# Kernel tuning notes

Measured on AMD Instinct MI355X. Metric: run time of the kernel, lower is better.

Reference implementation:

```python
import jax, jax.numpy as jnp
import numpy as np

N = 50000
E = 1600000
IN_CH = 128
HID = 32
HEADS = 4
NEG_SLOPE = 0.2
BN_EPS = 1e-5


def _gat_layer(x, src, dst, W, att_src, att_dst, n):
    """PyG-style GATConv (no bias; bias added by caller).
    x: [n, f_in], W: [f_in, heads*out], att_*: [heads, out].
    Returns [n, heads, out]."""
    heads, out_ch = att_src.shape
    h = (x @ W).reshape(n, heads, out_ch)                 # node projections
    a_s = jnp.einsum('nhc,hc->nh', h, att_src)            # per-node src logit
    a_d = jnp.einsum('nhc,hc->nh', h, att_dst)            # per-node dst logit
    e = jax.nn.leaky_relu(a_s[src] + a_d[dst], NEG_SLOPE)  # [E_tot, heads]
    m = jax.ops.segment_max(e, dst, num_segments=n)       # per-target max (stable softmax)
    ex = jnp.exp(e - m[dst])
    denom = jax.ops.segment_sum(ex, dst, num_segments=n)
    alpha = ex / denom[dst]                               # segment softmax over incoming edges
    out = jax.ops.segment_sum(h[src] * alpha[:, :, None], dst, num_segments=n)
    return out


def setup_inputs():
    key = jax.random.key(0)
    ks = jax.random.split(key, 8)
    x = jax.random.normal(ks[0], (N, IN_CH), dtype=jnp.float32)
    edge_index = jax.random.randint(ks[1], (2, E), 0, N, dtype=jnp.int32)
    s1 = 1.0 / float(np.sqrt(IN_CH))
    W1 = jax.random.uniform(ks[2], (IN_CH, HEADS * HID), jnp.float32, -s1, s1)
    att_src1 = jax.random.uniform(ks[3], (HEADS, HID), jnp.float32, -s1, s1)
    att_dst1 = jax.random.uniform(ks[4], (HEADS, HID), jnp.float32, -s1, s1)
    bias1 = jnp.zeros((HEADS * HID,), jnp.float32)
    bn_gamma = jnp.ones((HEADS * HID,), jnp.float32)
    bn_beta = jnp.zeros((HEADS * HID,), jnp.float32)
    bn_mean = jnp.zeros((HEADS * HID,), jnp.float32)
    bn_var = jnp.ones((HEADS * HID,), jnp.float32)
    s2 = 1.0 / float(np.sqrt(HEADS * HID))
    W2 = jax.random.uniform(ks[5], (HEADS * HID, 2), jnp.float32, -s2, s2)
    att_src2 = jax.random.uniform(ks[6], (1, 2), jnp.float32, -s2, s2)
    att_dst2 = jax.random.uniform(ks[7], (1, 2), jnp.float32, -s2, s2)
    bias2 = jnp.zeros((2,), jnp.float32)
    return {"x": x, "edge_index": edge_index, "W1": W1, "att_src1": att_src1,
            "att_dst1": att_dst1, "bias1": bias1, "bn_gamma": bn_gamma,
            "bn_beta": bn_beta, "bn_mean": bn_mean, "bn_var": bn_var,
            "W2": W2, "att_src2": att_src2, "att_dst2": att_dst2, "bias2": bias2}


def reference(x, edge_index, W1, att_src1, att_dst1, bias1, bn_gamma, bn_beta,
              bn_mean, bn_var, W2, att_src2, att_dst2, bias2):
    n = x.shape[0]
    # PyG GATConv default add_self_loops=True
    loop = jnp.arange(n, dtype=edge_index.dtype)
    src = jnp.concatenate([edge_index[0], loop])
    dst = jnp.concatenate([edge_index[1], loop])
    # conv1 (concat=True) + bias
    h1 = _gat_layer(x, src, dst, W1, att_src1, att_dst1, n).reshape(n, -1) + bias1
    # BatchNorm1d (eval mode, running stats)
    h1 = bn_gamma * (h1 - bn_mean) / jnp.sqrt(bn_var + BN_EPS) + bn_beta
    h1 = jax.nn.leaky_relu(h1, NEG_SLOPE)
    # dropout is identity in eval mode
    # conv2 (heads=1, concat=False -> mean over heads) + bias
    h2 = _gat_layer(h1, src, dst, W2, att_src2, att_dst2, n).mean(axis=1) + bias2
    return jax.nn.log_softmax(h2, axis=1)
```

## Files before the change

### kernel.cpp

```cpp
#include <hip/hip_runtime.h>
#include <math.h>

#define NN 50000
#define EE 1600000
#define FIN 128
#define FOUT 128
#define NEG 0.2f
#define BNEPS 1e-5f

#define NPART 8
#define PSZ (NN / NPART)

#define SCB 49
#define BEB 1024
#define NBUCK ((EE + BEB - 1) / BEB)
#define GGRP 8
#define BCAPG 30000
#define DSUB 8

#define XS_STRIDE 132
__global__ __launch_bounds__(256) void k_proj(const float* __restrict__ x,
    const float* __restrict__ W1, const float* __restrict__ asw, const float* __restrict__ adw,
    signed char* __restrict__ h8, float* __restrict__ hscale,
    float* __restrict__ as1, float* __restrict__ ad1) {
  __shared__ float xs[64 * XS_STRIDE];
  int t = threadIdx.x;
  int nb = blockIdx.x * 64;

  #pragma unroll
  for (int j = 0; j < 8; ++j) {
    int idx = t + 256 * j;
    int r = idx >> 5;
    int c4 = idx & 31;
    int n = nb + r; if (n >= NN) n = NN - 1;
    float4 v = *(const float4*)(x + (size_t)n * FIN + c4 * 4);
    *(float4*)(&xs[r * XS_STRIDE + c4 * 4]) = v;
  }
  __syncthreads();

  int cg = t & 15;
  int ng = t >> 4;
  int c0 = cg * 8;

  float acc[4][8];
  #pragma unroll
  for (int i = 0; i < 4; ++i)
    #pragma unroll
    for (int j = 0; j < 8; ++j) acc[i][j] = 0.f;

  for (int k0 = 0; k0 < FIN; k0 += 4) {
    float xr[4][4];
    #pragma unroll
    for (int i = 0; i < 4; ++i)
      *(float4*)xr[i] = *(const float4*)&xs[(ng * 4 + i) * XS_STRIDE + k0];
    #pragma unroll
    for (int kk = 0; kk < 4; ++kk) {
      float4 w0 = *(const float4*)(W1 + (k0 + kk) * FOUT + c0);
      float4 w1 = *(const float4*)(W1 + (k0 + kk) * FOUT + c0 + 4);
      float wv[8] = {w0.x, w0.y, w0.z, w0.w, w1.x, w1.y, w1.z, w1.w};
      #pragma unroll
      for (int i = 0; i < 4; ++i) {
        float xv = xr[i][kk];
        #pragma unroll
        for (int j = 0; j < 8; ++j) acc[i][j] = fmaf(xv, wv[j], acc[i][j]);
      }
    }
  }

  int head = cg >> 2;
  float vs[4], vd[4], rmax[4];
  #pragma unroll
  for (int i = 0; i < 4; ++i) {
    float s = 0.f, d = 0.f, m = 0.f;
    #pragma unroll
    for (int j = 0; j < 8; ++j) {
      s = fmaf(acc[i][j], asw[c0 + j], s);
      d = fmaf(acc[i][j], adw[c0 + j], d);
      m = fmaxf(m, fabsf(acc[i][j]));
    }
    vs[i] = s; vd[i] = d; rmax[i] = m;
  }
  #pragma unroll
  for (int i = 0; i < 4; ++i) {
    rmax[i] = fmaxf(rmax[i], __shfl_xor(rmax[i], 1, 64));
    rmax[i] = fmaxf(rmax[i], __shfl_xor(rmax[i], 2, 64));
    rmax[i] = fmaxf(rmax[i], __shfl_xor(rmax[i], 4, 64));
    rmax[i] = fmaxf(rmax[i], __shfl_xor(rmax[i], 8, 64));
  }
  #pragma unroll
  for (int i = 0; i < 4; ++i) {
    int n = nb + ng * 4 + i;
    if (n >= NN) continue;
    float rm = fmaxf(rmax[i], 1e-30f);
    float inv = 127.f / rm;
    unsigned b[8];
    #pragma unroll
    for (int j = 0; j < 8; ++j) {
      float qf = fminf(127.f, fmaxf(-127.f, rintf(acc[i][j] * inv)));
      b[j] = (unsigned)((int)qf) & 0xffu;
    }
    uint2 pk;
    pk.x = b[0] | (b[1] << 8) | (b[2] << 16) | (b[3] << 24);
    pk.y = b[4] | (b[5] << 8) | (b[6] << 16) | (b[7] << 24);
    *(uint2*)(h8 + (size_t)n * FOUT + c0) = pk;
    if (cg == 0) hscale[n] = rm / 127.f;
  }
  #pragma unroll
  for (int i = 0; i < 4; ++i) {
    vs[i] += __shfl_xor(vs[i], 1, 64); vs[i] += __shfl_xor(vs[i], 2, 64);
    vd[i] += __shfl_xor(vd[i], 1, 64); vd[i] += __shfl_xor(vd[i], 2, 64);
  }
  if ((cg & 3) == 0) {
    #pragma unroll
    for (int i = 0; i < 4; ++i) {
      int n = nb + ng * 4 + i;
      if (n < NN) { as1[n * 4 + head] = vs[i]; ad1[n * 4 + head] = vd[i]; }
    }
  }
}

__global__ __launch_bounds__(256) void k_bucket(const int* __restrict__ ei,
    int* __restrict__ bcur, unsigned* __restrict__ bkt) {
  __shared__ int lcnt[NPART];
  __shared__ int gbase[NPART];
  int t = threadIdx.x;
  int g = blockIdx.x & (GGRP - 1);
  if (t < NPART) lcnt[t] = 0;
  __syncthreads();
  int e0 = blockIdx.x * BEB;
  int part[4]; int lslot[4]; unsigned pk[4];
  #pragma unroll
  for (int j = 0; j < 4; ++j) {
    int i = e0 + j * 256 + t;
    if (i < EE) {
      int s = ei[i];
      int d = ei[EE + i];
      int p = d / PSZ;
      part[j] = p;
      pk[j] = (unsigned)s | ((unsigned)(d - p * PSZ) << 17);
      lslot[j] = atomicAdd(&lcnt[p], 1);
    } else part[j] = -1;
  }
  __syncthreads();
  if (t < NPART) gbase[t] = atomicAdd(&bcur[(g * NPART + t) * 16], lcnt[t]);
  __syncthreads();
  #pragma unroll
  for (int j = 0; j < 4; ++j) {
    if (part[j] >= 0)
      bkt[(size_t)(g * NPART + part[j]) * BCAPG + gbase[part[j]] + lslot[j]] = pk[j];
  }
}

__global__ __launch_bounds__(1024) void k_deg(const int* __restrict__ bcur,
    const unsigned* __restrict__ bkt, int* __restrict__ degp) {
  __shared__ int lh[PSZ];
  int t = threadIdx.x;
  int part = blockIdx.x & (NPART - 1);
  int g    = blockIdx.x >> 3;
  for (int i = t; i < PSZ; i += 1024) lh[i] = 0;
  __syncthreads();
  int cnt = bcur[(g * NPART + part) * 16];
  const unsigned* b = bkt + (size_t)(g * NPART + part) * BCAPG;
  for (int i = t; i < cnt; i += 1024)
    atomicAdd(&lh[b[i] >> 17], 1);
  __syncthreads();
  int* dst = degp + ((size_t)part * DSUB + g) * PSZ;
  for (int i = t; i < PSZ; i += 1024) dst[i] = lh[i];
}

__global__ __launch_bounds__(1024) void k_scanA(const int* __restrict__ degp,
    int* __restrict__ cur, int* __restrict__ bsum) {
  __shared__ int sums[1024];
  int t = threadIdx.x;
  int idx = blockIdx.x * 1024 + t;
  int v = 0;
  if (idx < NN) {
    int p = idx / PSZ, l = idx - p * PSZ;
    v = 1;
    #pragma unroll
    for (int k = 0; k < DSUB; ++k)
      v += degp[((size_t)p * DSUB + k) * PSZ + l];
  }
  sums[t] = v; __syncthreads();
  #pragma unroll
  for (int off = 1; off < 1024; off <<= 1) {
    int u = (t >= off) ? sums[t - off] : 0;
    __syncthreads();
    sums[t] += u;
    __syncthreads();
  }
  if (idx < NN) cur[idx] = sums[t] - v;
  if (t == 1023) bsum[blockIdx.x] = sums[1023];
}

__global__ __launch_bounds__(1024) void k_scanB(const int* __restrict__ bsum,
    int* __restrict__ offs, int* __restrict__ cur) {
  int b = blockIdx.x;
  int t = threadIdx.x;
  int base = 0;
  for (int i = 0; i < SCB; ++i) base += (i < b) ? bsum[i] : 0;
  int idx = b * 1024 + t;
  if (idx < NN) {
    int v = cur[idx] + base;
    offs[idx] = v;
    cur[idx] = v;
  }
  if (b == SCB - 1 && t == 0) {
    int total = base;
    for (int i = b; i < SCB; ++i) total += bsum[i];
    offs[NN] = total;
  }
}

__global__ __launch_bounds__(1024) void k_scat3(const int* __restrict__ bcur,
    const unsigned* __restrict__ bkt, const int* __restrict__ offs,
    const int* __restrict__ degp, int* __restrict__ csr) {
  __shared__ int lcur[PSZ];
  int t = threadIdx.x;
  int p = blockIdx.x & (NPART - 1);
  int g = blockIdx.x >> 3;
  int nbase = p * PSZ;
  for (int i = t; i < PSZ; i += 1024) {
    int c = offs[nbase + i];
    for (int gp = 0; gp < g; ++gp)
      c += degp[((size_t)p * DSUB + gp) * PSZ + i];
    lcur[i] = c;
  }
  __syncthreads();
  int cnt = bcur[(g * NPART + p) * 16];
  const unsigned* b = bkt + (size_t)(g * NPART + p) * BCAPG;
  for (int i = t; i < cnt; i += 1024) {
    unsigned v = b[i];
    int pos = atomicAdd(&lcur[v >> 17], 1);
    csr[pos] = (int)(v & 0x1ffffu);
  }
  if (g == DSUB - 1) {
    __syncthreads();
    for (int i = t; i < PSZ; i += 1024)
      csr[lcur[i]] = nbase + i;
  }
}

__global__ __launch_bounds__(256) void k_agg1(
    const int* __restrict__ offs, const int* __restrict__ csr,
    const signed char* __restrict__ h8, const float* __restrict__ hscale,
    const float* __restrict__ as1, const float* __restrict__ ad1,
    const float* __restrict__ bias1, const float* __restrict__ gamma, const float* __restrict__ beta,
    const float* __restrict__ mean, const float* __restrict__ var,
    const float* __restrict__ W2, const float* __restrict__ asw2, const float* __restrict__ adw2,
    float* __restrict__ h2, float* __restrict__ as2, float* __restrict__ ad2) {
  __shared__ float wlds[4][2][16][4];
  int wid = threadIdx.x >> 6;
  int lane = threadIdx.x & 63;
  int n = blockIdx.x * 4 + wid;
  if (n >= NN) return;
  int r0 = offs[n], r1 = offs[n + 1];
  int hh = lane >> 4;
  int ej = lane & 15;
  bool selhi = hh >= 2;
  bool oddh = hh & 1;
  const unsigned short* hp = (const unsigned short*)h8;
  float4 adv = *(const float4*)(ad1 + n * 4);
  float adA = selhi ? adv.z : adv.x;
  float adB = selhi ? adv.w : adv.y;
  float adsel = oddh ? adB : adA;

  float acc0 = 0.f, acc1 = 0.f, denp = 0.f;

#define WSEL(AV, HS, EXV, WV)                                      \
  float EXV, WV;                                                   \
  {                                                                \
    float eA = selhi ? AV.z : AV.x;                                \
    float eB = selhi ? AV.w : AV.y;                                \
    float e = (oddh ? eB : eA) + adsel;                            \
    e = e > 0.f ? e : NEG * e;                                     \
    EXV = __expf(e);                                               \
    WV = EXV * HS;                                                 \
  }

#define AGG_BODY2(SVN, BUF, J)                                     \
  {                                                                \
    int s = __builtin_amdgcn_readlane(SVN, (J));                   \
    float w = wlds[wid][BUF][(J)][hh];                             \
    unsigned pv = hp[(size_t)s * 64 + lane];                       \
    int q0 = ((int)(pv << 24)) >> 24;                              \
    int q1 = ((int)(pv << 16)) >> 24;                              \
    acc0 = fmaf(w, (float)q0, acc0);                               \
    acc1 = fmaf(w, (float)q1, acc1);                               \
  }

  int base = r0;
  for (; base + 32 <= r1; base += 32) {
    int sv0 = csr[base + ej];
    int sv1 = csr[base + 16 + ej];
    float hs0 = hscale[sv0];
    float hs1 = hscale[sv1];
    float4 av0 = *(const float4*)(as1 + sv0 * 4);
    float4 av1 = *(const float4*)(as1 + sv1 * 4);
    WSEL(av0, hs0, ex0, w0)
    WSEL(av1, hs1, ex1, w1)
    denp += ex0 + ex1;
    wlds[wid][0][ej][hh] = w0;
    wlds[wid][1][ej][hh] = w1;
    #pragma unroll
    for (int j = 0; j < 16; ++j) AGG_BODY2(sv0, 0, j)
    #pragma unroll
    for (int j = 0; j < 16; ++j) AGG_BODY2(sv1, 1, j)
  }
  if (base + 16 <= r1) {
    int sv0 = csr[base + ej];
    float hs0 = hscale[sv0];
    float4 av0 = *(const float4*)(as1 + sv0 * 4);
    WSEL(av0, hs0, ex0, w0)
    denp += ex0;
    wlds[wid][0][ej][hh] = w0;
    #pragma unroll
    for (int j = 0; j < 16; ++j) AGG_BODY2(sv0, 0, j)
    base += 16;
  }
  int m = r1 - base;
  if (m > 0) {
    int sv0 = csr[base + (ej < m ? ej : 0)];
    float hs0 = hscale[sv0];
    float4 av0 = *(const float4*)(as1 + sv0 * 4);
    WSEL(av0, hs0, ex0, w0)
    if (ej < m) { denp += ex0; wlds[wid][0][ej][hh] = w0; }
    for (int j = 0; j < m; ++j) AGG_BODY2(sv0, 0, j)
  }

  denp += __shfl_xor(denp, 1, 64);
  denp += __shfl_xor(denp, 2, 64);
  denp += __shfl_xor(denp, 4, 64);
  denp += __shfl_xor(denp, 8, 64);
  float den = denp;

  int c0 = lane * 2, c1 = lane * 2 + 1;
  float inv = 1.f / den;
  float o0 = acc0 * inv + bias1[c0];
  float o1 = acc1 * inv + bias1[c1];
  o0 = gamma[c0] * (o0 - mean[c0]) * rsqrtf(var[c0] + BNEPS) + beta[c0];
  o1 = gamma[c1] * (o1 - mean[c1]) * rsqrtf(var[c1] + BNEPS) + beta[c1];
  o0 = o0 > 0.f ? o0 : NEG * o0;
  o1 = o1 > 0.f ? o1 : NEG * o1;

  float p0 = o0 * W2[c0 * 2 + 0] + o1 * W2[c1 * 2 + 0];
  float p1 = o0 * W2[c0 * 2 + 1] + o1 * W2[c1 * 2 + 1];
  #pragma unroll
  for (int mm = 32; mm >= 1; mm >>= 1) {
    p0 += __shfl_xor(p0, mm, 64);
    p1 += __shfl_xor(p1, mm, 64);
  }
  if (lane == 0) {
    h2[n * 2 + 0] = p0;
    h2[n * 2 + 1] = p1;
    as2[n] = p0 * asw2[0] + p1 * asw2[1];
    ad2[n] = p0 * adw2[0] + p1 * adw2[1];
  }
}

__global__ __launch_bounds__(256) void k_agg2(
    const int* __restrict__ offs, const int* __restrict__ csr,
    const float* __restrict__ h2, const float* __restrict__ as2, const float* __restrict__ ad2,
    const float* __restrict__ bias2, float* __restrict__ out) {
  int wid = threadIdx.x >> 6;
  int lane = threadIdx.x & 63;
  int n = blockIdx.x * 4 + wid;
  if (n >= NN) return;
  int r0 = offs[n], r1 = offs[n + 1];
  float ad = ad2[n];

  float den = 0.f, a0 = 0.f, a1 = 0.f;
  for (int i = r0 + lane; i < r1; i += 64) {
    int s = csr[i];
    float e = as2[s] + ad; e = e > 0.f ? e : NEG * e;
    float ex = __expf(e);
    float2 hv = *(const float2*)(h2 + s * 2);
    den += ex;
    a0 = fmaf(ex, hv.x, a0);
    a1 = fmaf(ex, hv.y, a1);
  }
  #pragma unroll
  for (int mm = 32; mm >= 1; mm >>= 1) {
    den += __shfl_xor(den, mm, 64);
    a0  += __shfl_xor(a0, mm, 64);
    a1  += __shfl_xor(a1, mm, 64);
  }
  if (lane == 0) {
    float o0 = a0 / den + bias2[0];
    float o1 = a1 / den + bias2[1];
    float mx = fmaxf(o0, o1);
    float lse = mx + logf(__expf(o0 - mx) + __expf(o1 - mx));
    out[n * 2 + 0] = o0 - lse;
    out[n * 2 + 1] = o1 - lse;
  }
}

extern "C" void kernel_launch(void* const* d_in, const int* in_sizes, int n_in,
                              void* d_out, int out_size, void* d_ws, size_t ws_size,
                              hipStream_t stream) {
  const float* x     = (const float*)d_in[0];
  const int*   ei    = (const int*)d_in[1];
  const float* W1    = (const float*)d_in[2];
  const float* asw1  = (const float*)d_in[3];
  const float* adw1  = (const float*)d_in[4];
  const float* bias1 = (const float*)d_in[5];
  const float* gamma = (const float*)d_in[6];
  const float* beta  = (const float*)d_in[7];
  const float* mean  = (const float*)d_in[8];
  const float* var   = (const float*)d_in[9];
  const float* W2    = (const float*)d_in[10];
  const float* asw2  = (const float*)d_in[11];
  const float* adw2  = (const float*)d_in[12];
  const float* bias2 = (const float*)d_in[13];
  float* out = (float*)d_out;

  char* ws = (char*)d_ws;
  size_t off = 0;
  auto alloc = [&](size_t bytes) {
    void* p = ws + off;
    off += (bytes + 255) & ~(size_t)255;
    return p;
  };
  signed char* h8 = (signed char*)alloc((size_t)NN * FOUT);
  float* hscale = (float*)alloc((size_t)NN * 4);
  float* as1  = (float*)alloc((size_t)NN * 4 * 4);
  float* ad1  = (float*)alloc((size_t)NN * 4 * 4);
  int*   degp = (int*)alloc((size_t)NPART * DSUB * PSZ * 4);
  int*   offs = (int*)alloc(((size_t)NN + 1) * 4);
  int*   cur  = (int*)alloc((size_t)NN * 4);
  int*   bsum = (int*)alloc((size_t)SCB * 4);
  int*   bcur = (int*)alloc((size_t)GGRP * NPART * 16 * 4);
  int*   csr  = (int*)alloc((size_t)(EE + NN) * 4);
  unsigned* bkt = (unsigned*)alloc((size_t)GGRP * NPART * BCAPG * 4);
  float* h2   = (float*)alloc((size_t)NN * 2 * 4);
  float* as2  = (float*)alloc((size_t)NN * 4);
  float* ad2  = (float*)alloc((size_t)NN * 4);
  (void)ws_size; (void)in_sizes; (void)n_in; (void)out_size;

  hipMemsetAsync(bcur, 0, (size_t)GGRP * NPART * 16 * 4, stream);
  k_proj   <<<(NN + 63) / 64, 256, 0, stream>>>(x, W1, asw1, adw1, h8, hscale, as1, ad1);
  k_bucket <<<NBUCK, 256, 0, stream>>>(ei, bcur, bkt);
  k_deg    <<<NPART * DSUB, 1024, 0, stream>>>(bcur, bkt, degp);
  k_scanA  <<<SCB, 1024, 0, stream>>>(degp, cur, bsum);
  k_scanB  <<<SCB, 1024, 0, stream>>>(bsum, offs, cur);
  k_scat3  <<<NPART * DSUB, 1024, 0, stream>>>(bcur, bkt, offs, degp, csr);
  k_agg1   <<<(NN + 3) / 4, 256, 0, stream>>>(offs, csr, h8, hscale, as1, ad1, bias1, gamma, beta,
                                              mean, var, W2, asw2, adw2, h2, as2, ad2);
  k_agg2   <<<(NN + 3) / 4, 256, 0, stream>>>(offs, csr, h2, as2, ad2, bias2, out);
}
```

Baseline: 187.0 us.

## Split wave into two half-waves aggregating alternate edges with 4-byte row gathers

The layer-1 aggregation kernel now splits each 64-lane wave into two 32-lane halves. Each half handles 16 of every 32 incoming edges and each lane loads 4 int8 features per edge as one 32-bit load instead of 2 via a 16-bit load. Attention weights and source indices are staged in LDS for all 32 edges at once, and the partial accumulators are combined across halves with a cross-half shuffle at the end. This halves the number of serialized gather iterations per chunk and widens the per-lane load, at the cost of more LDS traffic, extra shuffles for the denominator, and removal of the separate 16-edge remainder path.

```diff
diff --git a/kernel.cpp b/kernel.cpp
--- a/kernel.cpp
+++ b/kernel.cpp
@@ -249,104 +249,109 @@
     const float* __restrict__ mean, const float* __restrict__ var,
     const float* __restrict__ W2, const float* __restrict__ asw2, const float* __restrict__ adw2,
     float* __restrict__ h2, float* __restrict__ as2, float* __restrict__ ad2) {
-  __shared__ float wlds[4][2][16][4];
+  __shared__ int   slds[4][32];
+  __shared__ float wlds[4][32][4];
   int wid = threadIdx.x >> 6;
   int lane = threadIdx.x & 63;
   int n = blockIdx.x * 4 + wid;
   if (n >= NN) return;
   int r0 = offs[n], r1 = offs[n + 1];
-  int hh = lane >> 4;
-  int ej = lane & 15;
-  bool selhi = hh >= 2;
-  bool oddh = hh & 1;
-  const unsigned short* hp = (const unsigned short*)h8;
-  float4 adv = *(const float4*)(ad1 + n * 4);
-  float adA = selhi ? adv.z : adv.x;
-  float adB = selhi ? adv.w : adv.y;
-  float adsel = oddh ? adB : adA;
-
-  float acc0 = 0.f, acc1 = 0.f, denp = 0.f;
-
-#define WSEL(AV, HS, EXV, WV)                                      \
-  float EXV, WV;                                                   \
+  int l  = lane & 31;
+  int hf = lane >> 5;
+  int hh = l >> 3;
+  const signed char* hpb = h8;
+  float2 adv = *(const float2*)(ad1 + n * 4 + hf * 2);
+
+  float acc0 = 0.f, acc1 = 0.f, acc2 = 0.f, acc3 = 0.f;
+  float denp0 = 0.f, denp1 = 0.f;
+
+#define AGG_PRE(IDX, PRED)                                         \
   {                                                                \
-    float eA = selhi ? AV.z : AV.x;                                \
-    float eB = selhi ? AV.w : AV.y;                                \
-    float e = (oddh ? eB : eA) + adsel;                            \
-    e = e > 0.f ? e : NEG * e;                                     \
-    EXV = __expf(e);                                               \
-    WV = EXV * HS;                                                 \
-  }
-
-#define AGG_BODY2(SVN, BUF, J)                                     \
+    int sv = csr[(IDX)];                                           \
+    float hs = hscale[sv];                                         \
+    float2 av = *(const float2*)(as1 + sv * 4 + hf * 2);           \
+    float e0 = av.x + adv.x; e0 = e0 > 0.f ? e0 : NEG * e0;        \
+    float e1 = av.y + adv.y; e1 = e1 > 0.f ? e1 : NEG * e1;        \
+    float ex0 = __expf(e0), ex1 = __expf(e1);                      \
+    float w0 = ex0 * hs, w1 = ex1 * hs;                            \
+    if (PRED) { denp0 += ex0; denp1 += ex1; }                      \
+    wlds[wid][l][hf * 2]     = (PRED) ? w0 : 0.f;                  \
+    wlds[wid][l][hf * 2 + 1] = (PRED) ? w1 : 0.f;                  \
+    if (hf == 0) slds[wid][l] = sv;                                \
+  }
+
+#define AGG_BODY(J)                                                \
   {                                                                \
-    int s = __builtin_amdgcn_readlane(SVN, (J));                   \
-    float w = wlds[wid][BUF][(J)][hh];                             \
-    unsigned pv = hp[(size_t)s * 64 + lane];                       \
+    int s = slds[wid][hf * 16 + (J)];                              \
+    float w = wlds[wid][hf * 16 + (J)][hh];                        \
+    unsigned pv = *(const unsigned*)(hpb + (size_t)s * FOUT + l * 4); \
     int q0 = ((int)(pv << 24)) >> 24;                              \
     int q1 = ((int)(pv << 16)) >> 24;                              \
+    int q2 = ((int)(pv << 8)) >> 24;                               \
+    int q3 = ((int)pv) >> 24;                                      \
     acc0 = fmaf(w, (float)q0, acc0);                               \
     acc1 = fmaf(w, (float)q1, acc1);                               \
+    acc2 = fmaf(w, (float)q2, acc2);                               \
+    acc3 = fmaf(w, (float)q3, acc3);                               \
   }
 
   int base = r0;
   for (; base + 32 <= r1; base += 32) {
-    int sv0 = csr[base + ej];
-    int sv1 = csr[base + 16 + ej];
-    float hs0 = hscale[sv0];
-    float hs1 = hscale[sv1];
-    float4 av0 = *(const float4*)(as1 + sv0 * 4);
-    float4 av1 = *(const float4*)(as1 + sv1 * 4);
-    WSEL(av0, hs0, ex0, w0)
-    WSEL(av1, hs1, ex1, w1)
-    denp += ex0 + ex1;
-    wlds[wid][0][ej][hh] = w0;
-    wlds[wid][1][ej][hh] = w1;
-    #pragma unroll
-    for (int j = 0; j < 16; ++j) AGG_BODY2(sv0, 0, j)
-    #pragma unroll
-    for (int j = 0; j < 16; ++j) AGG_BODY2(sv1, 1, j)
-  }
-  if (base + 16 <= r1) {
-    int sv0 = csr[base + ej];
-    float hs0 = hscale[sv0];
-    float4 av0 = *(const float4*)(as1 + sv0 * 4);
-    WSEL(av0, hs0, ex0, w0)
-    denp += ex0;
-    wlds[wid][0][ej][hh] = w0;
-    #pragma unroll
-    for (int j = 0; j < 16; ++j) AGG_BODY2(sv0, 0, j)
-    base += 16;
+    AGG_PRE(base + l, true)
+    #pragma unroll
+    for (int j = 0; j < 16; ++j) AGG_BODY(j)
   }
   int m = r1 - base;
   if (m > 0) {
-    int sv0 = csr[base + (ej < m ? ej : 0)];
-    float hs0 = hscale[sv0];
-    float4 av0 = *(const float4*)(as1 + sv0 * 4);
-    WSEL(av0, hs0, ex0, w0)
-    if (ej < m) { denp += ex0; wlds[wid][0][ej][hh] = w0; }
-    for (int j = 0; j < m; ++j) AGG_BODY2(sv0, 0, j)
-  }
-
-  denp += __shfl_xor(denp, 1, 64);
-  denp += __shfl_xor(denp, 2, 64);
-  denp += __shfl_xor(denp, 4, 64);
-  denp += __shfl_xor(denp, 8, 64);
-  float den = denp;
-
-  int c0 = lane * 2, c1 = lane * 2 + 1;
+    AGG_PRE(base + (l < m ? l : m - 1), l < m)
+    int jmax = m < 16 ? m : 16;
+    for (int j = 0; j < jmax; ++j) AGG_BODY(j)
+  }
+
+  acc0 += __shfl_xor(acc0, 32, 64);
+  acc1 += __shfl_xor(acc1, 32, 64);
+  acc2 += __shfl_xor(acc2, 32, 64);
+  acc3 += __shfl_xor(acc3, 32, 64);
+
+  #pragma unroll
+  for (int mm = 16; mm >= 1; mm >>= 1) {
+    denp0 += __shfl_xor(denp0, mm, 64);
+    denp1 += __shfl_xor(denp1, mm, 64);
+  }
+  float dOA = __shfl_xor(denp0, 32, 64);
+  float dOB = __shfl_xor(denp1, 32, 64);
+  float den0 = hf ? dOA : denp0;
+  float den1 = hf ? dOB : denp1;
+  float den2 = hf ? denp0 : dOA;
+  float den3 = hf ? denp1 : dOB;
+  float den = (hh == 0) ? den0 : (hh == 1) ? den1 : (hh == 2) ? den2 : den3;
+
+  int c0 = l * 4;
   float inv = 1.f / den;
-  float o0 = acc0 * inv + bias1[c0];
-  float o1 = acc1 * inv + bias1[c1];
-  o0 = gamma[c0] * (o0 - mean[c0]) * rsqrtf(var[c0] + BNEPS) + beta[c0];
-  o1 = gamma[c1] * (o1 - mean[c1]) * rsqrtf(var[c1] + BNEPS) + beta[c1];
+  float4 bi = *(const float4*)(bias1 + c0);
+  float4 ga = *(const float4*)(gamma + c0);
+  float4 be = *(const float4*)(beta + c0);
+  float4 mu = *(const float4*)(mean + c0);
+  float4 va = *(const float4*)(var + c0);
+  float o0 = acc0 * inv + bi.x;
+  float o1 = acc1 * inv + bi.y;
+  float o2 = acc2 * inv + bi.z;
+  float o3 = acc3 * inv + bi.w;
+  o0 = ga.x * (o0 - mu.x) * rsqrtf(va.x + BNEPS) + be.x;
+  o1 = ga.y * (o1 - mu.y) * rsqrtf(va.y + BNEPS) + be.y;
+  o2 = ga.z * (o2 - mu.z) * rsqrtf(va.z + BNEPS) + be.z;
+  o3 = ga.w * (o3 - mu.w) * rsqrtf(va.w + BNEPS) + be.w;
   o0 = o0 > 0.f ? o0 : NEG * o0;
   o1 = o1 > 0.f ? o1 : NEG * o1;
-
-  float p0 = o0 * W2[c0 * 2 + 0] + o1 * W2[c1 * 2 + 0];
-  float p1 = o0 * W2[c0 * 2 + 1] + o1 * W2[c1 * 2 + 1];
-  #pragma unroll
-  for (int mm = 32; mm >= 1; mm >>= 1) {
+  o2 = o2 > 0.f ? o2 : NEG * o2;
+  o3 = o3 > 0.f ? o3 : NEG * o3;
+
+  float p0 = o0 * W2[(c0 + 0) * 2 + 0] + o1 * W2[(c0 + 1) * 2 + 0]
+           + o2 * W2[(c0 + 2) * 2 + 0] + o3 * W2[(c0 + 3) * 2 + 0];
+  float p1 = o0 * W2[(c0 + 0) * 2 + 1] + o1 * W2[(c0 + 1) * 2 + 1]
+           + o2 * W2[(c0 + 2) * 2 + 1] + o3 * W2[(c0 + 3) * 2 + 1];
+  #pragma unroll
+  for (int mm = 16; mm >= 1; mm >>= 1) {
     p0 += __shfl_xor(p0, mm, 64);
     p1 += __shfl_xor(p1, mm, 64);
   }
```

Result: faster. 169.4 us (-9.4%).
